# Kernel tuning notes

Hardware: AMD Instinct MI355X
Metric: run time of the kernel (lower is better)

Reference implementation:

```python
import jax, jax.numpy as jnp
import numpy as np

INPUT_SIZE = 128
HIDDEN = 64
OUTPUT = 64
T, B = 2048, 256


def setup_inputs() -> dict:
    key = jax.random.key(0)
    ks = jax.random.split(key, 8)
    s_ih = 1.0 / np.sqrt(HIDDEN)
    x = jax.random.normal(ks[0], (T, B, INPUT_SIZE), dtype=jnp.float32)
    # PyTorch nn.LSTM params: weight_ih [4H, in], weight_hh [4H, H], biases [4H]; gate order i,f,g,o
    W_ih = jax.random.uniform(ks[1], (4 * HIDDEN, INPUT_SIZE), minval=-s_ih, maxval=s_ih, dtype=jnp.float32)
    W_hh = jax.random.uniform(ks[2], (4 * HIDDEN, HIDDEN), minval=-s_ih, maxval=s_ih, dtype=jnp.float32)
    b_ih = jax.random.uniform(ks[3], (4 * HIDDEN,), minval=-s_ih, maxval=s_ih, dtype=jnp.float32)
    b_hh = jax.random.uniform(ks[4], (4 * HIDDEN,), minval=-s_ih, maxval=s_ih, dtype=jnp.float32)
    W_fc = jax.random.uniform(ks[5], (OUTPUT, HIDDEN), minval=-s_ih, maxval=s_ih, dtype=jnp.float32)
    b_fc = jax.random.uniform(ks[6], (OUTPUT,), minval=-s_ih, maxval=s_ih, dtype=jnp.float32)
    return {"x": x, "W_ih": W_ih, "W_hh": W_hh, "b_ih": b_ih, "b_hh": b_hh, "W_fc": W_fc, "b_fc": b_fc}


def _lstm_fc(x, W_ih, W_hh, b_ih, b_hh, W_fc, b_fc):
    H = W_hh.shape[1]
    # Precompute input contributions for all timesteps: [T, B, 4H]
    xg = jnp.einsum('tbi,gi->tbg', x, W_ih) + b_ih + b_hh

    def step(carry, xg_t):
        h, c = carry
        gates = xg_t + h @ W_hh.T  # [B, 4H]
        i = jax.nn.sigmoid(gates[:, 0 * H:1 * H])
        f = jax.nn.sigmoid(gates[:, 1 * H:2 * H])
        g = jnp.tanh(gates[:, 2 * H:3 * H])
        o = jax.nn.sigmoid(gates[:, 3 * H:4 * H])
        c_new = f * c + i * g
        h_new = o * jnp.tanh(c_new)
        return (h_new, c_new), h_new

    B = x.shape[1]
    h0 = jnp.zeros((B, H), dtype=x.dtype)
    c0 = jnp.zeros((B, H), dtype=x.dtype)
    _, hs = jax.lax.scan(step, (h0, c0), xg)  # hs: [T, B, H]
    return jnp.einsum('tbh,oh->tbo', hs, W_fc) + b_fc


def reference(x, W_ih, W_hh, b_ih, b_hh, W_fc, b_fc):
    return _lstm_fc(x, W_ih, W_hh, b_ih, b_hh, W_fc, b_fc)
```

## Files before the change

### kernel.cpp

```cpp
#include <hip/hip_runtime.h>


#define T_STEPS 2048
#define BATCH   256
#define INSZ    128
#define HID     64
#define G4      256

typedef __attribute__((ext_vector_type(8))) short bf16x8;
typedef __attribute__((ext_vector_type(4))) float f32x4;
typedef __attribute__((ext_vector_type(2))) _Float16 half2v;
typedef _Float16 __attribute__((may_alias)) half_a;

__device__ __forceinline__ short f2bf(float f) {
  unsigned u = __float_as_uint(f);
  unsigned r = (u + 0x7fffu + ((u >> 16) & 1u)) >> 16;
  return (short)r;
}
__device__ __forceinline__ float bf2f(short s) {
  return __uint_as_float(((unsigned)(unsigned short)s) << 16);
}
__device__ __forceinline__ float bf2f_u(unsigned short s) {
  return __uint_as_float(((unsigned)s) << 16);
}

#define LOG2E 1.44269504088896f
__device__ __forceinline__ float fast_sigmoid(float x) {
  float e = __builtin_amdgcn_exp2f(-LOG2E * x);
  return __builtin_amdgcn_rcpf(1.f + e);
}
__device__ __forceinline__ float fast_tanh(float x) {
  float e = __builtin_amdgcn_exp2f(-2.f * LOG2E * x);
  return fmaf(2.f, __builtin_amdgcn_rcpf(1.f + e), -1.f);
}

__device__ __forceinline__ f32x4 mfma16(bf16x8 a, bf16x8 b, f32x4 c) {
  return __builtin_amdgcn_mfma_f32_16x16x32_bf16(a, b, c, 0, 0, 0);
}

__device__ __forceinline__ float fdot2(unsigned hp, unsigned wp, float acc) {
#if __has_builtin(__builtin_amdgcn_fdot2)
  return __builtin_amdgcn_fdot2(__builtin_bit_cast(half2v, hp),
                                __builtin_bit_cast(half2v, wp), acc, false);
#else
  float d;
  asm("v_dot2_f32_f16 %0, %1, %2, %3" : "=v"(d) : "v"(hp), "v"(wp), "v"(acc));
  return d;
#endif
}
__device__ __forceinline__ unsigned pack_h2(float a, float b) {
  half2v p = {(_Float16)a, (_Float16)b};
  return __builtin_bit_cast(unsigned, p);
}

__global__ void prep_kernel(const float* __restrict__ W_ih,
                            const float* __restrict__ b_ih,
                            const float* __restrict__ b_hh,
                            short* __restrict__ Whi, short* __restrict__ Wlo,
                            float* __restrict__ bias) {
  int i = blockIdx.x * 256 + threadIdx.x;
  float w = W_ih[i];
  short h = f2bf(w);
  Whi[i] = h;
  Wlo[i] = f2bf(w - bf2f(h));
  if (i < G4) bias[i] = b_ih[i] + b_hh[i];
}

__global__ __launch_bounds__(256, 2) void phase1_kernel(
    const float* __restrict__ x, const short* __restrict__ Whi,
    const short* __restrict__ Wlo, const float* __restrict__ bias,
    short* __restrict__ xg) {
  int wave = threadIdx.x >> 6, lane = threadIdx.x & 63;
  int col = lane & 15, quad = lane >> 4;
  long rowbase = (long)blockIdx.x * 128 + wave * 32;

  bf16x8 Ah[2][4], Al[2][4];
#pragma unroll
  for (int rt = 0; rt < 2; ++rt) {
    const float* xp = x + (rowbase + rt * 16 + col) * INSZ + quad * 8;
#pragma unroll
    for (int kk = 0; kk < 4; ++kk) {
      float4 v0 = *(const float4*)(xp + kk * 32);
      float4 v1 = *(const float4*)(xp + kk * 32 + 4);
      bf16x8 hh, ll;
      float vv[8] = {v0.x, v0.y, v0.z, v0.w, v1.x, v1.y, v1.z, v1.w};
#pragma unroll
      for (int j = 0; j < 8; ++j) {
        short hb = f2bf(vv[j]);
        hh[j] = hb;
        ll[j] = f2bf(vv[j] - bf2f(hb));
      }
      Ah[rt][kk] = hh;
      Al[rt][kk] = ll;
    }
  }

#pragma unroll 1
  for (int gt = 0; gt < 16; ++gt) {
    int grow = gt * 16 + col;
    const short* bph = Whi + grow * INSZ + quad * 8;
    const short* bpl = Wlo + grow * INSZ + quad * 8;
    f32x4 acc0 = {0.f, 0.f, 0.f, 0.f}, acc1 = {0.f, 0.f, 0.f, 0.f};
#pragma unroll
    for (int kk = 0; kk < 4; ++kk) {
      bf16x8 bh = *(const bf16x8*)(bph + kk * 32);
      bf16x8 bl = *(const bf16x8*)(bpl + kk * 32);
      acc0 = mfma16(Ah[0][kk], bh, acc0);
      acc1 = mfma16(Ah[1][kk], bh, acc1);
      acc0 = mfma16(Al[0][kk], bh, acc0);
      acc1 = mfma16(Al[1][kk], bh, acc1);
      acc0 = mfma16(Ah[0][kk], bl, acc0);
      acc1 = mfma16(Ah[1][kk], bl, acc1);
    }
    float bv = bias[grow];
#pragma unroll
    for (int rt = 0; rt < 2; ++rt) {
      f32x4 a = rt ? acc1 : acc0;
#pragma unroll
      for (int r = 0; r < 4; ++r) {
        long m = rowbase + rt * 16 + quad * 4 + r;
        xg[m * G4 + grow] = f2bf(a[r] + bv);
      }
    }
  }
}

__global__ __launch_bounds__(64, 1) void lstm_fc_kernel(
    const short* __restrict__ xg, const float* __restrict__ W_hh,
    const float* __restrict__ W_fc, const float* __restrict__ b_fc,
    float* __restrict__ out) {
  int b = blockIdx.x, j = threadIdx.x;
  __shared__ uint4 hbuf[2][8];

  unsigned whh[4][32];
#pragma unroll
  for (int g = 0; g < 4; ++g) {
    const float* wr = W_hh + (g * HID + j) * HID;
#pragma unroll
    for (int k = 0; k < 32; ++k) whh[g][k] = pack_h2(wr[2 * k], wr[2 * k + 1]);
  }
  unsigned wfc[32];
  {
    const float* fr = W_fc + j * HID;
#pragma unroll
    for (int k = 0; k < 32; ++k) wfc[k] = pack_h2(fr[2 * k], fr[2 * k + 1]);
  }
  float bfc = b_fc[j];

  if (j < 8) hbuf[0][j] = make_uint4(0, 0, 0, 0);

  const unsigned short* xq = (const unsigned short*)xg + (size_t)b * G4 + j;
  const unsigned short* pf = xq + 2 * (size_t)(BATCH * G4);
  unsigned short L0[4], L1[4];
#pragma unroll
  for (int g = 0; g < 4; ++g) {
    L0[g] = xq[g * HID];
    L1[g] = xq[(size_t)(BATCH * G4) + g * HID];
  }

  float* op = out + (size_t)b * HID + j;
  float c = 0.f;

  for (int t = 0; t < T_STEPS; ++t) {
    float a0 = bf2f_u(L0[0]), a1 = bf2f_u(L0[1]);
    float a2 = bf2f_u(L0[2]), a3 = bf2f_u(L0[3]);

    const uint4* hb = hbuf[t & 1];
    unsigned hp[32];
#pragma unroll
    for (int i = 0; i < 8; ++i) {
      uint4 v = hb[i];
      hp[4 * i + 0] = v.x; hp[4 * i + 1] = v.y;
      hp[4 * i + 2] = v.z; hp[4 * i + 3] = v.w;
    }

#pragma unroll
    for (int k = 0; k < 32; ++k) {
      a0 = fdot2(hp[k], whh[0][k], a0);
      a1 = fdot2(hp[k], whh[1][k], a1);
      a2 = fdot2(hp[k], whh[2][k], a2);
      a3 = fdot2(hp[k], whh[3][k], a3);
    }

#pragma unroll
    for (int g = 0; g < 4; ++g) L0[g] = L1[g];
    if (t + 2 < T_STEPS) {
#pragma unroll
      for (int g = 0; g < 4; ++g) L1[g] = pf[g * HID];
      pf += BATCH * G4;
    }

    float iv = fast_sigmoid(a0);
    float fv = fast_sigmoid(a1);
    float gv = fast_tanh(a2);
    float ov = fast_sigmoid(a3);
    c = fmaf(fv, c, iv * gv);
    float h = ov * fast_tanh(c);

    ((half_a*)hbuf[(t + 1) & 1])[j] = (_Float16)h;

    float f0 = 0.f, f1 = 0.f, f2 = 0.f, f3 = 0.f;
#pragma unroll
    for (int k = 0; k < 8; ++k) {
      f0 = fdot2(hp[4 * k + 0], wfc[4 * k + 0], f0);
      f1 = fdot2(hp[4 * k + 1], wfc[4 * k + 1], f1);
      f2 = fdot2(hp[4 * k + 2], wfc[4 * k + 2], f2);
      f3 = fdot2(hp[4 * k + 3], wfc[4 * k + 3], f3);
    }
    if (t > 0) {
      op[0] = ((f0 + f1) + (f2 + f3)) + bfc;
      op += BATCH * HID;
    }
  }

  {
    const uint4* hb = hbuf[T_STEPS & 1];
    float f0 = 0.f, f1 = 0.f, f2 = 0.f, f3 = 0.f;
#pragma unroll
    for (int i = 0; i < 8; ++i) {
      uint4 v = hb[i];
      f0 = fdot2(v.x, wfc[4 * i + 0], f0);
      f1 = fdot2(v.y, wfc[4 * i + 1], f1);
      f2 = fdot2(v.z, wfc[4 * i + 2], f2);
      f3 = fdot2(v.w, wfc[4 * i + 3], f3);
    }
    op[0] = ((f0 + f1) + (f2 + f3)) + bfc;
  }
}

extern "C" void kernel_launch(void* const* d_in, const int* in_sizes, int n_in,
                              void* d_out, int out_size, void* d_ws, size_t ws_size,
                              hipStream_t stream) {
  const float* x    = (const float*)d_in[0];
  const float* W_ih = (const float*)d_in[1];
  const float* W_hh = (const float*)d_in[2];
  const float* b_ih = (const float*)d_in[3];
  const float* b_hh = (const float*)d_in[4];
  const float* W_fc = (const float*)d_in[5];
  const float* b_fc = (const float*)d_in[6];
  float* out = (float*)d_out;

  char* ws = (char*)d_ws;
  short* Whi  = (short*)ws;
  short* Wlo  = (short*)(ws + 65536);
  float* bias = (float*)(ws + 131072);
  short* xg   = (short*)(ws + 132096);

  prep_kernel<<<128, 256, 0, stream>>>(W_ih, b_ih, b_hh, Whi, Wlo, bias);
  phase1_kernel<<<4096, 256, 0, stream>>>(x, Whi, Wlo, bias, xg);
  lstm_fc_kernel<<<BATCH, 64, 0, stream>>>(xg, W_hh, W_fc, b_fc, out);
}
```

Baseline: 1.631 ms.

## Use f16 MFMA for LSTM recurrence with 16-batch blocks and fragment-ordered xg

```diff
diff --git a/kernel.cpp b/kernel.cpp
--- a/kernel.cpp
+++ b/kernel.cpp
@@ -9,8 +9,9 @@
 
 typedef __attribute__((ext_vector_type(8))) short bf16x8;
 typedef __attribute__((ext_vector_type(4))) float f32x4;
-typedef __attribute__((ext_vector_type(2))) _Float16 half2v;
-typedef _Float16 __attribute__((may_alias)) half_a;
+typedef __attribute__((ext_vector_type(8))) _Float16 f16x8;
+typedef f16x8 __attribute__((may_alias)) f16x8_a;
+typedef __attribute__((ext_vector_type(4))) short s16x4;
 
 __device__ __forceinline__ short f2bf(float f) {
   unsigned u = __float_as_uint(f);
@@ -20,8 +21,11 @@
 __device__ __forceinline__ float bf2f(short s) {
   return __uint_as_float(((unsigned)(unsigned short)s) << 16);
 }
-__device__ __forceinline__ float bf2f_u(unsigned short s) {
-  return __uint_as_float(((unsigned)s) << 16);
+__device__ __forceinline__ float bflo(unsigned u) {
+  return __uint_as_float(u << 16);
+}
+__device__ __forceinline__ float bfhi(unsigned u) {
+  return __uint_as_float(u & 0xffff0000u);
 }
 
 #define LOG2E 1.44269504088896f
@@ -37,20 +41,8 @@
 __device__ __forceinline__ f32x4 mfma16(bf16x8 a, bf16x8 b, f32x4 c) {
   return __builtin_amdgcn_mfma_f32_16x16x32_bf16(a, b, c, 0, 0, 0);
 }
-
-__device__ __forceinline__ float fdot2(unsigned hp, unsigned wp, float acc) {
-#if __has_builtin(__builtin_amdgcn_fdot2)
-  return __builtin_amdgcn_fdot2(__builtin_bit_cast(half2v, hp),
-                                __builtin_bit_cast(half2v, wp), acc, false);
-#else
-  float d;
-  asm("v_dot2_f32_f16 %0, %1, %2, %3" : "=v"(d) : "v"(hp), "v"(wp), "v"(acc));
-  return d;
-#endif
-}
-__device__ __forceinline__ unsigned pack_h2(float a, float b) {
-  half2v p = {(_Float16)a, (_Float16)b};
-  return __builtin_bit_cast(unsigned, p);
+__device__ __forceinline__ f32x4 mfma_f16(f16x8 a, f16x8 b, f32x4 c) {
+  return __builtin_amdgcn_mfma_f32_16x16x32_f16(a, b, c, 0, 0, 0);
 }
 
 __global__ void prep_kernel(const float* __restrict__ W_ih,
@@ -95,9 +87,13 @@
     }
   }
 
+  const long t = rowbase >> 8;
+  const int Bk0 = (int)((rowbase & 255) >> 4);
+
 #pragma unroll 1
-  for (int gt = 0; gt < 16; ++gt) {
-    int grow = gt * 16 + col;
+  for (int idx = 0; idx < 16; ++idx) {
+    int w4 = idx >> 2, tt = idx & 3;
+    int grow = (tt * 4 + w4) * 16 + col;
     const short* bph = Whi + grow * INSZ + quad * 8;
     const short* bpl = Wlo + grow * INSZ + quad * 8;
     f32x4 acc0 = {0.f, 0.f, 0.f, 0.f}, acc1 = {0.f, 0.f, 0.f, 0.f};
@@ -113,119 +109,144 @@
       acc1 = mfma16(Ah[1][kk], bl, acc1);
     }
     float bv = bias[grow];
-#pragma unroll
-    for (int rt = 0; rt < 2; ++rt) {
-      f32x4 a = rt ? acc1 : acc0;
-#pragma unroll
-      for (int r = 0; r < 4; ++r) {
-        long m = rowbase + rt * 16 + quad * 4 + r;
-        xg[m * G4 + grow] = f2bf(a[r] + bv);
-      }
-    }
-  }
-}
-
-__global__ __launch_bounds__(64, 1) void lstm_fc_kernel(
+    s16x4 v0, v1;
+#pragma unroll
+    for (int r = 0; r < 4; ++r) {
+      v0[r] = f2bf(acc0[r] + bv);
+      v1[r] = f2bf(acc1[r] + bv);
+    }
+    size_t e0 =
+        ((((size_t)t * 16 + Bk0) * 4 + (size_t)w4) * 64 + lane) * 16 + tt * 4;
+    *(s16x4*)(xg + e0) = v0;
+    *(s16x4*)(xg + e0 + 4096) = v1;
+  }
+}
+
+__global__ __launch_bounds__(256, 1) void lstm_fc_kernel(
     const short* __restrict__ xg, const float* __restrict__ W_hh,
     const float* __restrict__ W_fc, const float* __restrict__ b_fc,
     float* __restrict__ out) {
-  int b = blockIdx.x, j = threadIdx.x;
-  __shared__ uint4 hbuf[2][8];
-
-  unsigned whh[4][32];
-#pragma unroll
-  for (int g = 0; g < 4; ++g) {
-    const float* wr = W_hh + (g * HID + j) * HID;
-#pragma unroll
-    for (int k = 0; k < 32; ++k) whh[g][k] = pack_h2(wr[2 * k], wr[2 * k + 1]);
-  }
-  unsigned wfc[32];
+  const int tid = threadIdx.x;
+  const int L = tid & 63, w = tid >> 6;
+  const int col = L & 15, quad = L >> 4;
+  const int Bk = blockIdx.x;
+
+  __shared__ alignas(16) char hmem[2][2048];
+
+  f16x8 whhB[4][2];
+#pragma unroll
+  for (int tt = 0; tt < 4; ++tt) {
+    const float* wr = W_hh + (tt * 64 + 16 * w + col) * HID + quad * 8;
+#pragma unroll
+    for (int kh = 0; kh < 2; ++kh) {
+      f16x8 f;
+#pragma unroll
+      for (int j = 0; j < 8; ++j) f[j] = (_Float16)wr[kh * 32 + j];
+      whhB[tt][kh] = f;
+    }
+  }
+  f16x8 wfcB[2];
   {
-    const float* fr = W_fc + j * HID;
-#pragma unroll
-    for (int k = 0; k < 32; ++k) wfc[k] = pack_h2(fr[2 * k], fr[2 * k + 1]);
-  }
-  float bfc = b_fc[j];
-
-  if (j < 8) hbuf[0][j] = make_uint4(0, 0, 0, 0);
-
-  const unsigned short* xq = (const unsigned short*)xg + (size_t)b * G4 + j;
-  const unsigned short* pf = xq + 2 * (size_t)(BATCH * G4);
-  unsigned short L0[4], L1[4];
-#pragma unroll
-  for (int g = 0; g < 4; ++g) {
-    L0[g] = xq[g * HID];
-    L1[g] = xq[(size_t)(BATCH * G4) + g * HID];
-  }
-
-  float* op = out + (size_t)b * HID + j;
-  float c = 0.f;
-
-  for (int t = 0; t < T_STEPS; ++t) {
-    float a0 = bf2f_u(L0[0]), a1 = bf2f_u(L0[1]);
-    float a2 = bf2f_u(L0[2]), a3 = bf2f_u(L0[3]);
-
-    const uint4* hb = hbuf[t & 1];
-    unsigned hp[32];
-#pragma unroll
-    for (int i = 0; i < 8; ++i) {
-      uint4 v = hb[i];
-      hp[4 * i + 0] = v.x; hp[4 * i + 1] = v.y;
-      hp[4 * i + 2] = v.z; hp[4 * i + 3] = v.w;
-    }
-
-#pragma unroll
-    for (int k = 0; k < 32; ++k) {
-      a0 = fdot2(hp[k], whh[0][k], a0);
-      a1 = fdot2(hp[k], whh[1][k], a1);
-      a2 = fdot2(hp[k], whh[2][k], a2);
-      a3 = fdot2(hp[k], whh[3][k], a3);
-    }
-
-#pragma unroll
-    for (int g = 0; g < 4; ++g) L0[g] = L1[g];
-    if (t + 2 < T_STEPS) {
-#pragma unroll
-      for (int g = 0; g < 4; ++g) L1[g] = pf[g * HID];
-      pf += BATCH * G4;
-    }
-
-    float iv = fast_sigmoid(a0);
-    float fv = fast_sigmoid(a1);
-    float gv = fast_tanh(a2);
-    float ov = fast_sigmoid(a3);
-    c = fmaf(fv, c, iv * gv);
-    float h = ov * fast_tanh(c);
-
-    ((half_a*)hbuf[(t + 1) & 1])[j] = (_Float16)h;
-
-    float f0 = 0.f, f1 = 0.f, f2 = 0.f, f3 = 0.f;
-#pragma unroll
-    for (int k = 0; k < 8; ++k) {
-      f0 = fdot2(hp[4 * k + 0], wfc[4 * k + 0], f0);
-      f1 = fdot2(hp[4 * k + 1], wfc[4 * k + 1], f1);
-      f2 = fdot2(hp[4 * k + 2], wfc[4 * k + 2], f2);
-      f3 = fdot2(hp[4 * k + 3], wfc[4 * k + 3], f3);
-    }
-    if (t > 0) {
-      op[0] = ((f0 + f1) + (f2 + f3)) + bfc;
-      op += BATCH * HID;
-    }
-  }
-
+    const float* fr = W_fc + (16 * w + col) * HID + quad * 8;
+#pragma unroll
+    for (int kh = 0; kh < 2; ++kh) {
+      f16x8 f;
+#pragma unroll
+      for (int j = 0; j < 8; ++j) f[j] = (_Float16)fr[kh * 32 + j];
+      wfcB[kh] = f;
+    }
+  }
+  float bfc = b_fc[16 * w + col];
+  f32x4 fbias = {bfc, bfc, bfc, bfc};
+
+  const int rd_off = (col * 128 + quad * 16) ^ ((col & 7) << 4);
+  const int rd_off1 = rd_off ^ 64;
+  int wr_off[4];
+#pragma unroll
+  for (int r = 0; r < 4; ++r) {
+    int b = quad * 4 + r;
+    wr_off[r] = (b * 128 + (16 * w + col) * 2) ^ ((b & 7) << 4);
+  }
+
+  *(float4*)(&hmem[0][0] + tid * 16) = make_float4(0.f, 0.f, 0.f, 0.f);
+
+  const short* xp = xg + (((size_t)Bk * 4 + w) * 64 + L) * 16;
+  uint4 xs[4][2];
+#pragma unroll
+  for (int s = 0; s < 4; ++s) {
+    xs[s][0] = *(const uint4*)(xp + (size_t)s * 65536);
+    xs[s][1] = *(const uint4*)(xp + (size_t)s * 65536 + 8);
+  }
+  const short* xnext = xp + (size_t)4 * 65536;
+
+  float* outp = out + ((size_t)Bk * 16 + quad * 4) * 64 + 16 * w + col;
+
+  float cst[4] = {0.f, 0.f, 0.f, 0.f};
+
+  __syncthreads();
+
+#define LSTM_STEP(S, PF)                                                   \
+  {                                                                        \
+    const int sp = (S) & 1;                                                \
+    const char* rb = hmem[sp];                                             \
+    f16x8 na0 = *(const f16x8_a*)(rb + rd_off);                            \
+    f16x8 na1 = *(const f16x8_a*)(rb + rd_off1);                           \
+    uint4 xa = xs[(S)][0], xb = xs[(S)][1];                                \
+    f32x4 g0 = {bflo(xa.x), bfhi(xa.x), bflo(xa.y), bfhi(xa.y)};           \
+    f32x4 g1 = {bflo(xa.z), bfhi(xa.z), bflo(xa.w), bfhi(xa.w)};           \
+    f32x4 g2 = {bflo(xb.x), bfhi(xb.x), bflo(xb.y), bfhi(xb.y)};           \
+    f32x4 g3 = {bflo(xb.z), bfhi(xb.z), bflo(xb.w), bfhi(xb.w)};           \
+    g0 = mfma_f16(na0, whhB[0][0], g0);                                    \
+    g1 = mfma_f16(na0, whhB[1][0], g1);                                    \
+    g2 = mfma_f16(na0, whhB[2][0], g2);                                    \
+    g3 = mfma_f16(na0, whhB[3][0], g3);                                    \
+    g0 = mfma_f16(na1, whhB[0][1], g0);                                    \
+    g1 = mfma_f16(na1, whhB[1][1], g1);                                    \
+    g2 = mfma_f16(na1, whhB[2][1], g2);                                    \
+    g3 = mfma_f16(na1, whhB[3][1], g3);                                    \
+    if (PF) {                                                              \
+      xs[(S)][0] = *(const uint4*)(xnext);                                 \
+      xs[(S)][1] = *(const uint4*)(xnext + 8);                             \
+      xnext += 65536;                                                      \
+    }                                                                      \
+    f32x4 fcv = mfma_f16(na0, wfcB[0], fbias);                             \
+    fcv = mfma_f16(na1, wfcB[1], fcv);                                     \
+    if (t + (S) > 0) {                                                     \
+      float* o = outp + (size_t)(t + (S)-1) * 16384;                       \
+      o[0] = fcv[0]; o[64] = fcv[1]; o[128] = fcv[2]; o[192] = fcv[3];     \
+    }                                                                      \
+    char* wb = hmem[sp ^ 1];                                               \
+    _Pragma("unroll") for (int r = 0; r < 4; ++r) {                        \
+      float iv = fast_sigmoid(g0[r]);                                      \
+      float fv = fast_sigmoid(g1[r]);                                      \
+      float gv = fast_tanh(g2[r]);                                         \
+      float ov = fast_sigmoid(g3[r]);                                      \
+      cst[r] = fmaf(fv, cst[r], iv * gv);                                  \
+      float hv = ov * fast_tanh(cst[r]);                                   \
+      *(_Float16*)(wb + wr_off[r]) = (_Float16)hv;                         \
+    }                                                                      \
+    __builtin_amdgcn_sched_barrier(0);                                     \
+    asm volatile("s_waitcnt lgkmcnt(0)" ::: "memory");  \
+    __builtin_amdgcn_s_barrier();                       \
+    __builtin_amdgcn_sched_barrier(0);                                     \
+  }
+
+  for (int t = 0; t < T_STEPS - 4; t += 4) {
+    LSTM_STEP(0, 1) LSTM_STEP(1, 1) LSTM_STEP(2, 1) LSTM_STEP(3, 1)
+  }
   {
-    const uint4* hb = hbuf[T_STEPS & 1];
-    float f0 = 0.f, f1 = 0.f, f2 = 0.f, f3 = 0.f;
-#pragma unroll
-    for (int i = 0; i < 8; ++i) {
-      uint4 v = hb[i];
-      f0 = fdot2(v.x, wfc[4 * i + 0], f0);
-      f1 = fdot2(v.y, wfc[4 * i + 1], f1);
-      f2 = fdot2(v.z, wfc[4 * i + 2], f2);
-      f3 = fdot2(v.w, wfc[4 * i + 3], f3);
-    }
-    op[0] = ((f0 + f1) + (f2 + f3)) + bfc;
-  }
+    const int t = T_STEPS - 4;
+    LSTM_STEP(0, 0) LSTM_STEP(1, 0) LSTM_STEP(2, 0) LSTM_STEP(3, 0)
+  }
+  {
+    f16x8 fa0 = *(const f16x8_a*)(hmem[0] + rd_off);
+    f16x8 fa1 = *(const f16x8_a*)(hmem[0] + rd_off1);
+    f32x4 fcv = mfma_f16(fa0, wfcB[0], fbias);
+    fcv = mfma_f16(fa1, wfcB[1], fcv);
+    float* o = outp + (size_t)(T_STEPS - 1) * 16384;
+    o[0] = fcv[0]; o[64] = fcv[1]; o[128] = fcv[2]; o[192] = fcv[3];
+  }
+#undef LSTM_STEP
 }
 
 extern "C" void kernel_launch(void* const* d_in, const int* in_sizes, int n_in,
@@ -248,5 +269,5 @@
 
   prep_kernel<<<128, 256, 0, stream>>>(W_ih, b_ih, b_hh, Whi, Wlo, bias);
   phase1_kernel<<<4096, 256, 0, stream>>>(x, Whi, Wlo, bias, xg);
-  lstm_fc_kernel<<<BATCH, 64, 0, stream>>>(xg, W_hh, W_fc, b_fc, out);
-}
+  lstm_fc_kernel<<<16, 256, 0, stream>>>(xg, W_hh, W_fc, b_fc, out);
+}
```

Measured after the change: 1.809 ms. 1.11x slower.
